# Performance work log

Measured on AMD Instinct MI355X. Metric: run time of the kernel, lower is better.

## Reference

```python
import jax, jax.numpy as jnp
import numpy as np

N_NODES = 100000
N_EDGES = 3200000
D = 256


def setup_inputs() -> dict:
    key = jax.random.key(0)
    k1, k2, k3, k4, k5, k6 = jax.random.split(key, 6)
    embeddings = jax.random.normal(k1, (N_NODES, D), dtype=jnp.float32)
    edge_vals = jax.random.uniform(k2, (N_EDGES,), dtype=jnp.float32)
    # glorot-ish scale for the dense transforms
    scale = 1.0 / np.sqrt(D)
    W1 = jax.random.normal(k3, (D, D), dtype=jnp.float32) * scale
    W2 = jax.random.normal(k4, (D, D), dtype=jnp.float32) * scale
    edge_rows = jax.random.randint(k5, (N_EDGES,), 0, N_NODES, dtype=jnp.int32)
    edge_cols = jax.random.randint(k6, (N_EDGES,), 0, N_NODES, dtype=jnp.int32)
    return {
        "embeddings": embeddings,
        "edge_vals": edge_vals,
        "W1": W1,
        "W2": W2,
        "edge_rows": edge_rows,
        "edge_cols": edge_cols,
    }


def reference(embeddings, edge_vals, W1, W2, edge_rows, edge_cols):
    # SpMM: neighbor_interaction = A @ embeddings, A given as COO (rows, cols, vals)
    gathered = edge_vals[:, None] * embeddings[edge_cols]          # [E, D]
    neighbor = jax.ops.segment_sum(gathered, edge_rows,
                                   num_segments=embeddings.shape[0])  # [N, D]
    # include_self_messages = True branch:
    # self_interaction + neighbor_messages  ==  (emb + neighbor) @ W1
    out = (embeddings + neighbor) @ W1 + (neighbor * embeddings) @ W2
    return out
```

## Files before the change

### kernel.cpp

```cpp
#include <hip/hip_runtime.h>
#include <cstdint>
#include <cstddef>

#define N_NODES 100000
#define N_EDGES 3200000
#define DD 256
#define KK 512
#define MPAD 100096
#define NSCAN 98
#define NGRP 8
#define GRP_ROWS 12500
#define NSLOT 256
#define SLOT_E 12500

typedef __attribute__((ext_vector_type(8))) __bf16 bf16x8;
typedef __attribute__((ext_vector_type(4))) __bf16 bf16x4;
typedef __attribute__((ext_vector_type(4))) float f32x4;

__device__ __forceinline__ void gload_lds16(const void* gsrc, void* lds) {
  __builtin_amdgcn_global_load_lds((const __attribute__((address_space(1))) void*)gsrc,
                                   (__attribute__((address_space(3))) void*)lds,
                                   16, 0, 0);
}


__global__ void conve_kernel(const float* __restrict__ emb, __bf16* __restrict__ embB) {
  int i = blockIdx.x * blockDim.x + threadIdx.x;
  float4 v = ((const float4*)emb)[i];
  bf16x4 o;
  o[0] = (__bf16)v.x; o[1] = (__bf16)v.y; o[2] = (__bf16)v.z; o[3] = (__bf16)v.w;
  ((bf16x4*)embB)[i] = o;
}

__global__ void convw_kernel(const float* __restrict__ W1, const float* __restrict__ W2,
                             __bf16* __restrict__ Wt) {
  int idx = blockIdx.x * blockDim.x + threadIdx.x;
  int n = idx >> 9;
  int k = idx & 511;
  float v = (k < 256) ? W1[k * 256 + n] : W2[(k - 256) * 256 + n];
  Wt[idx] = (__bf16)v;
}


__global__ void zero_ints_kernel(int* __restrict__ p, int n) {
  int i = blockIdx.x * blockDim.x + threadIdx.x;
  if (i < n) p[i] = 0;
}

__global__ void hist_kernel(const int* __restrict__ rows, int* __restrict__ counts, int e) {
  int i = blockIdx.x * blockDim.x + threadIdx.x;
  int stride = gridDim.x * blockDim.x;
  for (; i < e; i += stride) atomicAdd(&counts[rows[i]], 1);
}

__global__ void scan_block_kernel(const int* __restrict__ counts, int* __restrict__ offsets,
                                  int* __restrict__ blockSums, int n) {
  __shared__ int s[1024];
  int t = threadIdx.x;
  int i = blockIdx.x * 1024 + t;
  int v = (i < n) ? counts[i] : 0;
  s[t] = v;
  __syncthreads();
  for (int off = 1; off < 1024; off <<= 1) {
    int x = (t >= off) ? s[t - off] : 0;
    __syncthreads();
    s[t] += x;
    __syncthreads();
  }
  if (i < n) offsets[i + 1] = s[t];
  if (t == 1023) blockSums[blockIdx.x] = s[1023];
}

__global__ void scan_sums_kernel(const int* __restrict__ blockSums, int* __restrict__ blockBase,
                                 int nb, int* __restrict__ offsets) {
  __shared__ int s[128];
  int t = threadIdx.x;
  int v = (t < nb) ? blockSums[t] : 0;
  s[t] = v;
  __syncthreads();
  for (int off = 1; off < 128; off <<= 1) {
    int x = (t >= off) ? s[t - off] : 0;
    __syncthreads();
    s[t] += x;
    __syncthreads();
  }
  if (t < nb) blockBase[t] = s[t] - v;
  if (t == 0) offsets[0] = 0;
}

__global__ void scan_add_kernel(const int* __restrict__ counts, int* __restrict__ offsets,
                                const int* __restrict__ blockBase, int* __restrict__ cursor, int n) {
  int i = blockIdx.x * 1024 + threadIdx.x;
  if (i < n) {
    int incl = offsets[i + 1] + blockBase[blockIdx.x];
    offsets[i + 1] = incl;
    cursor[i] = incl - counts[i];
  }
}

__global__ void bin_kernel(const int* __restrict__ rows, const int* __restrict__ cols,
                           const float* __restrict__ vals, int* __restrict__ cursor,
                           uint2* __restrict__ sedge) {
  const int g = blockIdx.x & (NGRP - 1);
  const int s = blockIdx.x >> 3;
  const int rlo = g * GRP_ROWS;
  const int rhi = rlo + GRP_ROWS;
  const int base = s * SLOT_E;
  for (int i = base + threadIdx.x; i < base + SLOT_E; i += 256) {
    int r = rows[i];
    if (r >= rlo && r < rhi) {
      int pos = atomicAdd(&cursor[r], 1);
      sedge[pos] = make_uint2((unsigned)cols[i], __float_as_uint(vals[i]));
    }
  }
}


__global__ void spmm_fuse_kernel(const __bf16* __restrict__ embB, const int* __restrict__ offsets,
                                 const uint2* __restrict__ sedge, __bf16* __restrict__ X) {
  int gw = (blockIdx.x << 2) + (threadIdx.x >> 6);
  int lane = threadIdx.x & 63;
  bf16x4* xp1 = (bf16x4*)(X + (size_t)gw * KK + 4 * lane);
  bf16x4* xp2 = (bf16x4*)(X + (size_t)gw * KK + DD + 4 * lane);
  if (gw >= N_NODES) {
    bf16x4 z;
    z[0] = (__bf16)0.f; z[1] = (__bf16)0.f; z[2] = (__bf16)0.f; z[3] = (__bf16)0.f;
    *xp1 = z; *xp2 = z;
    return;
  }
  const bf16x4* ev = (const bf16x4*)embB;
  float ax = 0.f, ay = 0.f, az = 0.f, aw = 0.f;
  int e = offsets[gw];
  const int eend = offsets[gw + 1];
  for (; e + 3 < eend; e += 4) {
    uint2 e0 = sedge[e], e1 = sedge[e + 1], e2 = sedge[e + 2], e3 = sedge[e + 3];
    float v0 = __uint_as_float(e0.y), v1 = __uint_as_float(e1.y);
    float v2 = __uint_as_float(e2.y), v3 = __uint_as_float(e3.y);
    bf16x4 x0 = ev[(size_t)e0.x * 64 + lane];
    bf16x4 x1 = ev[(size_t)e1.x * 64 + lane];
    bf16x4 x2 = ev[(size_t)e2.x * 64 + lane];
    bf16x4 x3 = ev[(size_t)e3.x * 64 + lane];
    ax = fmaf(v0, (float)x0[0], ax); ay = fmaf(v0, (float)x0[1], ay);
    az = fmaf(v0, (float)x0[2], az); aw = fmaf(v0, (float)x0[3], aw);
    ax = fmaf(v1, (float)x1[0], ax); ay = fmaf(v1, (float)x1[1], ay);
    az = fmaf(v1, (float)x1[2], az); aw = fmaf(v1, (float)x1[3], aw);
    ax = fmaf(v2, (float)x2[0], ax); ay = fmaf(v2, (float)x2[1], ay);
    az = fmaf(v2, (float)x2[2], az); aw = fmaf(v2, (float)x2[3], aw);
    ax = fmaf(v3, (float)x3[0], ax); ay = fmaf(v3, (float)x3[1], ay);
    az = fmaf(v3, (float)x3[2], az); aw = fmaf(v3, (float)x3[3], aw);
  }
  for (; e < eend; ++e) {
    uint2 ee = sedge[e];
    float v = __uint_as_float(ee.y);
    bf16x4 x = ev[(size_t)ee.x * 64 + lane];
    ax = fmaf(v, (float)x[0], ax); ay = fmaf(v, (float)x[1], ay);
    az = fmaf(v, (float)x[2], az); aw = fmaf(v, (float)x[3], aw);
  }
  bf16x4 er = ev[(size_t)gw * 64 + lane];
  float ex = (float)er[0], ey = (float)er[1], ez = (float)er[2], ew = (float)er[3];
  bf16x4 o1, o2;
  o1[0] = (__bf16)(ex + ax); o1[1] = (__bf16)(ey + ay);
  o1[2] = (__bf16)(ez + az); o1[3] = (__bf16)(ew + aw);
  o2[0] = (__bf16)(ex * ax); o2[1] = (__bf16)(ey * ay);
  o2[2] = (__bf16)(ez * az); o2[3] = (__bf16)(ew * aw);
  *xp1 = o1;
  *xp2 = o2;
}


__global__ __launch_bounds__(256) void gemm_kernel(const __bf16* __restrict__ X,
                                                   const __bf16* __restrict__ Wt,
                                                   float* __restrict__ out) {
  __shared__ __align__(16) __bf16 As[128 * 64];
  __shared__ __align__(16) __bf16 Bs[128 * 64];
  const int t = threadIdx.x;
  const int w = t >> 6, lane = t & 63;
  const int m0 = blockIdx.x * 128;
  const int n0 = blockIdx.y * 128;
  const int wm = (w >> 1) * 64, wn = (w & 1) * 64;
  const int lrow = lane >> 3, lcol = lane & 7;

  f32x4 acc[4][4];
#pragma unroll
  for (int i = 0; i < 4; ++i)
#pragma unroll
    for (int j = 0; j < 4; ++j) {
      f32x4 z = {0.f, 0.f, 0.f, 0.f};
      acc[i][j] = z;
    }

  for (int kt = 0; kt < KK; kt += 64) {
#pragma unroll
    for (int q = 0; q < 4; ++q) {
      const int cbase = w * 256 + q * 64;
      const int arow = m0 + w * 32 + q * 8 + lrow;
      gload_lds16(X + (size_t)arow * KK + kt + lcol * 8, (char*)As + cbase * 16);
      const int brow = n0 + w * 32 + q * 8 + lrow;
      gload_lds16(Wt + (size_t)brow * KK + kt + lcol * 8, (char*)Bs + cbase * 16);
    }
    __syncthreads();
#pragma unroll
    for (int kk = 0; kk < 64; kk += 32) {
      const int ko = kk + (lane >> 4) * 8;
      bf16x8 af[4], bg[4];
#pragma unroll
      for (int i = 0; i < 4; ++i)
        af[i] = *(const bf16x8*)(As + (wm + i * 16 + (lane & 15)) * 64 + ko);
#pragma unroll
      for (int j = 0; j < 4; ++j)
        bg[j] = *(const bf16x8*)(Bs + (wn + j * 16 + (lane & 15)) * 64 + ko);
#pragma unroll
      for (int i = 0; i < 4; ++i)
#pragma unroll
        for (int j = 0; j < 4; ++j)
          acc[i][j] = __builtin_amdgcn_mfma_f32_16x16x32_bf16(af[i], bg[j], acc[i][j], 0, 0, 0);
    }
    __syncthreads();
  }

  const int orow0 = m0 + wm + ((lane >> 4) << 2);
  const int ocol0 = n0 + wn + (lane & 15);
#pragma unroll
  for (int i = 0; i < 4; ++i)
#pragma unroll
    for (int j = 0; j < 4; ++j)
#pragma unroll
      for (int r = 0; r < 4; ++r) {
        const int row = orow0 + i * 16 + r;
        if (row < N_NODES) out[(size_t)row * DD + ocol0 + j * 16] = acc[i][j][r];
      }
}


extern "C" void kernel_launch(void* const* d_in, const int* in_sizes, int n_in,
                              void* d_out, int out_size, void* d_ws, size_t ws_size,
                              hipStream_t stream) {
  const float* emb  = (const float*)d_in[0];
  const float* ev   = (const float*)d_in[1];
  const float* W1   = (const float*)d_in[2];
  const float* W2   = (const float*)d_in[3];
  const int* erows  = (const int*)d_in[4];
  const int* ecols  = (const int*)d_in[5];
  float* out = (float*)d_out;
  char* ws = (char*)d_ws;

  const size_t OFF_X   = 0;
  const size_t OFF_EMB = OFF_X   + (size_t)MPAD * KK * 2;
  const size_t OFF_WT  = OFF_EMB + (size_t)N_NODES * DD * 2;
  const size_t OFF_CNT = OFF_WT  + (size_t)KK * DD * 2;
  const size_t OFF_OFS = OFF_CNT + 401408;
  const size_t OFF_CUR = OFF_OFS + 401408;
  const size_t OFF_BS  = OFF_CUR + 401408;
  const size_t OFF_BB  = OFF_BS  + 4096;
  const size_t OFF_SE  = OFF_BB  + 4096;

  __bf16* X     = (__bf16*)(ws + OFF_X);
  __bf16* embB  = (__bf16*)(ws + OFF_EMB);
  __bf16* Wt    = (__bf16*)(ws + OFF_WT);
  int* counts   = (int*)(ws + OFF_CNT);
  int* offsets  = (int*)(ws + OFF_OFS);
  int* cursor   = (int*)(ws + OFF_CUR);
  int* bsums    = (int*)(ws + OFF_BS);
  int* bbase    = (int*)(ws + OFF_BB);
  uint2* sedge  = (uint2*)(ws + OFF_SE);

  conve_kernel<<<(N_NODES * 64) / 256, 256, 0, stream>>>(emb, embB);
  convw_kernel<<<(KK * DD) / 256, 256, 0, stream>>>(W1, W2, Wt);

  zero_ints_kernel<<<(N_NODES + 255) / 256, 256, 0, stream>>>(counts, N_NODES);
  hist_kernel<<<2048, 256, 0, stream>>>(erows, counts, N_EDGES);
  scan_block_kernel<<<NSCAN, 1024, 0, stream>>>(counts, offsets, bsums, N_NODES);
  scan_sums_kernel<<<1, 128, 0, stream>>>(bsums, bbase, NSCAN, offsets);
  scan_add_kernel<<<NSCAN, 1024, 0, stream>>>(counts, offsets, bbase, cursor, N_NODES);
  bin_kernel<<<NGRP * NSLOT, 256, 0, stream>>>(erows, ecols, ev, cursor, sedge);

  spmm_fuse_kernel<<<MPAD / 4, 256, 0, stream>>>(embB, offsets, sedge, X);

  gemm_kernel<<<dim3(MPAD / 128, 2), 256, 0, stream>>>(X, Wt, out);

  (void)in_sizes; (void)n_in; (void)out_size; (void)ws_size;
}
```

Measured before the change: 770.5 us.

## Fuse SpMM aggregation with the dense GEMM through a swizzled LDS tile

New measurement: 852.6 us. +10.7%, slower.

```diff
diff --git a/kernel.cpp b/kernel.cpp
--- a/kernel.cpp
+++ b/kernel.cpp
@@ -17,12 +17,6 @@
 typedef __attribute__((ext_vector_type(4))) __bf16 bf16x4;
 typedef __attribute__((ext_vector_type(4))) float f32x4;
 
-__device__ __forceinline__ void gload_lds16(const void* gsrc, void* lds) {
-  __builtin_amdgcn_global_load_lds((const __attribute__((address_space(1))) void*)gsrc,
-                                   (__attribute__((address_space(3))) void*)lds,
-                                   16, 0, 0);
-}
-
 
 __global__ void conve_kernel(const float* __restrict__ emb, __bf16* __restrict__ embB) {
   int i = blockIdx.x * blockDim.x + threadIdx.x;
@@ -47,10 +41,16 @@
   if (i < n) p[i] = 0;
 }
 
-__global__ void hist_kernel(const int* __restrict__ rows, int* __restrict__ counts, int e) {
-  int i = blockIdx.x * blockDim.x + threadIdx.x;
-  int stride = gridDim.x * blockDim.x;
-  for (; i < e; i += stride) atomicAdd(&counts[rows[i]], 1);
+__global__ void hist_kernel(const int* __restrict__ rows, int* __restrict__ counts) {
+  const int g = blockIdx.x & (NGRP - 1);
+  const int s = blockIdx.x >> 3;
+  const int rlo = g * GRP_ROWS;
+  const int rhi = rlo + GRP_ROWS;
+  const int base = s * SLOT_E;
+  for (int i = base + threadIdx.x; i < base + SLOT_E; i += 256) {
+    int r = rows[i];
+    if (r >= rlo && r < rhi) atomicAdd(&counts[r], 1);
+  }
 }
 
 __global__ void scan_block_kernel(const int* __restrict__ counts, int* __restrict__ offsets,
@@ -116,118 +116,107 @@
 }
 
 
-__global__ void spmm_fuse_kernel(const __bf16* __restrict__ embB, const int* __restrict__ offsets,
-                                 const uint2* __restrict__ sedge, __bf16* __restrict__ X) {
-  int gw = (blockIdx.x << 2) + (threadIdx.x >> 6);
-  int lane = threadIdx.x & 63;
-  bf16x4* xp1 = (bf16x4*)(X + (size_t)gw * KK + 4 * lane);
-  bf16x4* xp2 = (bf16x4*)(X + (size_t)gw * KK + DD + 4 * lane);
-  if (gw >= N_NODES) {
-    bf16x4 z;
-    z[0] = (__bf16)0.f; z[1] = (__bf16)0.f; z[2] = (__bf16)0.f; z[3] = (__bf16)0.f;
-    *xp1 = z; *xp2 = z;
-    return;
-  }
-  const bf16x4* ev = (const bf16x4*)embB;
-  float ax = 0.f, ay = 0.f, az = 0.f, aw = 0.f;
-  int e = offsets[gw];
-  const int eend = offsets[gw + 1];
-  for (; e + 3 < eend; e += 4) {
-    uint2 e0 = sedge[e], e1 = sedge[e + 1], e2 = sedge[e + 2], e3 = sedge[e + 3];
-    float v0 = __uint_as_float(e0.y), v1 = __uint_as_float(e1.y);
-    float v2 = __uint_as_float(e2.y), v3 = __uint_as_float(e3.y);
-    bf16x4 x0 = ev[(size_t)e0.x * 64 + lane];
-    bf16x4 x1 = ev[(size_t)e1.x * 64 + lane];
-    bf16x4 x2 = ev[(size_t)e2.x * 64 + lane];
-    bf16x4 x3 = ev[(size_t)e3.x * 64 + lane];
-    ax = fmaf(v0, (float)x0[0], ax); ay = fmaf(v0, (float)x0[1], ay);
-    az = fmaf(v0, (float)x0[2], az); aw = fmaf(v0, (float)x0[3], aw);
-    ax = fmaf(v1, (float)x1[0], ax); ay = fmaf(v1, (float)x1[1], ay);
-    az = fmaf(v1, (float)x1[2], az); aw = fmaf(v1, (float)x1[3], aw);
-    ax = fmaf(v2, (float)x2[0], ax); ay = fmaf(v2, (float)x2[1], ay);
-    az = fmaf(v2, (float)x2[2], az); aw = fmaf(v2, (float)x2[3], aw);
-    ax = fmaf(v3, (float)x3[0], ax); ay = fmaf(v3, (float)x3[1], ay);
-    az = fmaf(v3, (float)x3[2], az); aw = fmaf(v3, (float)x3[3], aw);
-  }
-  for (; e < eend; ++e) {
-    uint2 ee = sedge[e];
-    float v = __uint_as_float(ee.y);
-    bf16x4 x = ev[(size_t)ee.x * 64 + lane];
-    ax = fmaf(v, (float)x[0], ax); ay = fmaf(v, (float)x[1], ay);
-    az = fmaf(v, (float)x[2], az); aw = fmaf(v, (float)x[3], aw);
-  }
-  bf16x4 er = ev[(size_t)gw * 64 + lane];
-  float ex = (float)er[0], ey = (float)er[1], ez = (float)er[2], ew = (float)er[3];
-  bf16x4 o1, o2;
-  o1[0] = (__bf16)(ex + ax); o1[1] = (__bf16)(ey + ay);
-  o1[2] = (__bf16)(ez + az); o1[3] = (__bf16)(ew + aw);
-  o2[0] = (__bf16)(ex * ax); o2[1] = (__bf16)(ey * ay);
-  o2[2] = (__bf16)(ez * az); o2[3] = (__bf16)(ew * aw);
-  *xp1 = o1;
-  *xp2 = o2;
-}
-
-
-__global__ __launch_bounds__(256) void gemm_kernel(const __bf16* __restrict__ X,
-                                                   const __bf16* __restrict__ Wt,
-                                                   float* __restrict__ out) {
-  __shared__ __align__(16) __bf16 As[128 * 64];
-  __shared__ __align__(16) __bf16 Bs[128 * 64];
+__global__ __launch_bounds__(256) void spmm_gemm_kernel(
+    const __bf16* __restrict__ embB, const int* __restrict__ offsets,
+    const uint2* __restrict__ sedge, const __bf16* __restrict__ Wt,
+    float* __restrict__ out) {
+  __shared__ __align__(16) char Xs[32 * 1024];
   const int t = threadIdx.x;
   const int w = t >> 6, lane = t & 63;
-  const int m0 = blockIdx.x * 128;
-  const int n0 = blockIdx.y * 128;
-  const int wm = (w >> 1) * 64, wn = (w & 1) * 64;
-  const int lrow = lane >> 3, lcol = lane & 7;
-
-  f32x4 acc[4][4];
-#pragma unroll
-  for (int i = 0; i < 4; ++i)
+  const int m0 = blockIdx.x * 32;
+  const bf16x4* ev = (const bf16x4*)embB;
+
+  for (int rr = 0; rr < 8; ++rr) {
+    const int lr = (w << 3) + rr;
+    const int r = m0 + lr;
+    const int sw = (lr & 7) << 4;
+    bf16x4* q1 = (bf16x4*)(Xs + lr * 1024 + ((lane * 8) ^ sw));
+    bf16x4* q2 = (bf16x4*)(Xs + lr * 1024 + ((512 + lane * 8) ^ sw));
+    if (r >= N_NODES) {
+      bf16x4 z;
+      z[0] = (__bf16)0.f; z[1] = (__bf16)0.f; z[2] = (__bf16)0.f; z[3] = (__bf16)0.f;
+      *q1 = z; *q2 = z;
+      continue;
+    }
+    float ax = 0.f, ay = 0.f, az = 0.f, aw = 0.f;
+    int e = offsets[r];
+    const int eend = offsets[r + 1];
+    for (; e + 3 < eend; e += 4) {
+      uint2 e0 = sedge[e], e1 = sedge[e + 1], e2 = sedge[e + 2], e3 = sedge[e + 3];
+      float v0 = __uint_as_float(e0.y), v1 = __uint_as_float(e1.y);
+      float v2 = __uint_as_float(e2.y), v3 = __uint_as_float(e3.y);
+      bf16x4 x0 = ev[(size_t)e0.x * 64 + lane];
+      bf16x4 x1 = ev[(size_t)e1.x * 64 + lane];
+      bf16x4 x2 = ev[(size_t)e2.x * 64 + lane];
+      bf16x4 x3 = ev[(size_t)e3.x * 64 + lane];
+      ax = fmaf(v0, (float)x0[0], ax); ay = fmaf(v0, (float)x0[1], ay);
+      az = fmaf(v0, (float)x0[2], az); aw = fmaf(v0, (float)x0[3], aw);
+      ax = fmaf(v1, (float)x1[0], ax); ay = fmaf(v1, (float)x1[1], ay);
+      az = fmaf(v1, (float)x1[2], az); aw = fmaf(v1, (float)x1[3], aw);
+      ax = fmaf(v2, (float)x2[0], ax); ay = fmaf(v2, (float)x2[1], ay);
+      az = fmaf(v2, (float)x2[2], az); aw = fmaf(v2, (float)x2[3], aw);
+      ax = fmaf(v3, (float)x3[0], ax); ay = fmaf(v3, (float)x3[1], ay);
+      az = fmaf(v3, (float)x3[2], az); aw = fmaf(v3, (float)x3[3], aw);
+    }
+    for (; e < eend; ++e) {
+      uint2 ee = sedge[e];
+      float v = __uint_as_float(ee.y);
+      bf16x4 x = ev[(size_t)ee.x * 64 + lane];
+      ax = fmaf(v, (float)x[0], ax); ay = fmaf(v, (float)x[1], ay);
+      az = fmaf(v, (float)x[2], az); aw = fmaf(v, (float)x[3], aw);
+    }
+    bf16x4 er = ev[(size_t)r * 64 + lane];
+    float ex = (float)er[0], ey = (float)er[1], ez = (float)er[2], ew = (float)er[3];
+    bf16x4 o1, o2;
+    o1[0] = (__bf16)(ex + ax); o1[1] = (__bf16)(ey + ay);
+    o1[2] = (__bf16)(ez + az); o1[3] = (__bf16)(ew + aw);
+    o2[0] = (__bf16)(ex * ax); o2[1] = (__bf16)(ey * ay);
+    o2[2] = (__bf16)(ez * az); o2[3] = (__bf16)(ew * aw);
+    *q1 = o1;
+    *q2 = o2;
+  }
+  __syncthreads();
+
+  f32x4 acc[2][4];
+#pragma unroll
+  for (int mt = 0; mt < 2; ++mt)
 #pragma unroll
     for (int j = 0; j < 4; ++j) {
       f32x4 z = {0.f, 0.f, 0.f, 0.f};
-      acc[i][j] = z;
-    }
-
-  for (int kt = 0; kt < KK; kt += 64) {
-#pragma unroll
-    for (int q = 0; q < 4; ++q) {
-      const int cbase = w * 256 + q * 64;
-      const int arow = m0 + w * 32 + q * 8 + lrow;
-      gload_lds16(X + (size_t)arow * KK + kt + lcol * 8, (char*)As + cbase * 16);
-      const int brow = n0 + w * 32 + q * 8 + lrow;
-      gload_lds16(Wt + (size_t)brow * KK + kt + lcol * 8, (char*)Bs + cbase * 16);
-    }
-    __syncthreads();
-#pragma unroll
-    for (int kk = 0; kk < 64; kk += 32) {
-      const int ko = kk + (lane >> 4) * 8;
-      bf16x8 af[4], bg[4];
-#pragma unroll
-      for (int i = 0; i < 4; ++i)
-        af[i] = *(const bf16x8*)(As + (wm + i * 16 + (lane & 15)) * 64 + ko);
+      acc[mt][j] = z;
+    }
+  const int n0w = w << 6;
+  const int l15 = lane & 15, lhi = lane >> 4;
+#pragma unroll 4
+  for (int ks = 0; ks < 16; ++ks) {
+    const int kk = ks << 5;
+    bf16x8 af[2], bg[4];
+#pragma unroll
+    for (int mt = 0; mt < 2; ++mt) {
+      const int ar = (mt << 4) + l15;
+      int off = ar * 1024 + (kk << 1) + (lhi << 4);
+      off ^= (ar & 7) << 4;
+      af[mt] = *(const bf16x8*)(Xs + off);
+    }
+#pragma unroll
+    for (int j = 0; j < 4; ++j)
+      bg[j] = *(const bf16x8*)(Wt + (size_t)(n0w + (j << 4) + l15) * KK + kk + (lhi << 3));
+#pragma unroll
+    for (int mt = 0; mt < 2; ++mt)
 #pragma unroll
       for (int j = 0; j < 4; ++j)
-        bg[j] = *(const bf16x8*)(Bs + (wn + j * 16 + (lane & 15)) * 64 + ko);
-#pragma unroll
-      for (int i = 0; i < 4; ++i)
-#pragma unroll
-        for (int j = 0; j < 4; ++j)
-          acc[i][j] = __builtin_amdgcn_mfma_f32_16x16x32_bf16(af[i], bg[j], acc[i][j], 0, 0, 0);
-    }
-    __syncthreads();
-  }
-
-  const int orow0 = m0 + wm + ((lane >> 4) << 2);
-  const int ocol0 = n0 + wn + (lane & 15);
-#pragma unroll
-  for (int i = 0; i < 4; ++i)
+        acc[mt][j] = __builtin_amdgcn_mfma_f32_16x16x32_bf16(af[mt], bg[j], acc[mt][j], 0, 0, 0);
+  }
+
+  const int ocol0 = n0w + l15;
+#pragma unroll
+  for (int mt = 0; mt < 2; ++mt)
 #pragma unroll
     for (int j = 0; j < 4; ++j)
 #pragma unroll
-      for (int r = 0; r < 4; ++r) {
-        const int row = orow0 + i * 16 + r;
-        if (row < N_NODES) out[(size_t)row * DD + ocol0 + j * 16] = acc[i][j][r];
+      for (int r2 = 0; r2 < 4; ++r2) {
+        const int row = m0 + (mt << 4) + (lhi << 2) + r2;
+        if (row < N_NODES) out[(size_t)row * DD + ocol0 + (j << 4)] = acc[mt][j][r2];
       }
 }
 
@@ -244,8 +233,7 @@
   float* out = (float*)d_out;
   char* ws = (char*)d_ws;
 
-  const size_t OFF_X   = 0;
-  const size_t OFF_EMB = OFF_X   + (size_t)MPAD * KK * 2;
+  const size_t OFF_EMB = 0;
   const size_t OFF_WT  = OFF_EMB + (size_t)N_NODES * DD * 2;
   const size_t OFF_CNT = OFF_WT  + (size_t)KK * DD * 2;
   const size_t OFF_OFS = OFF_CNT + 401408;
@@ -254,7 +242,6 @@
   const size_t OFF_BB  = OFF_BS  + 4096;
   const size_t OFF_SE  = OFF_BB  + 4096;
 
-  __bf16* X     = (__bf16*)(ws + OFF_X);
   __bf16* embB  = (__bf16*)(ws + OFF_EMB);
   __bf16* Wt    = (__bf16*)(ws + OFF_WT);
   int* counts   = (int*)(ws + OFF_CNT);
@@ -268,15 +255,13 @@
   convw_kernel<<<(KK * DD) / 256, 256, 0, stream>>>(W1, W2, Wt);
 
   zero_ints_kernel<<<(N_NODES + 255) / 256, 256, 0, stream>>>(counts, N_NODES);
-  hist_kernel<<<2048, 256, 0, stream>>>(erows, counts, N_EDGES);
+  hist_kernel<<<NGRP * NSLOT, 256, 0, stream>>>(erows, counts);
   scan_block_kernel<<<NSCAN, 1024, 0, stream>>>(counts, offsets, bsums, N_NODES);
   scan_sums_kernel<<<1, 128, 0, stream>>>(bsums, bbase, NSCAN, offsets);
   scan_add_kernel<<<NSCAN, 1024, 0, stream>>>(counts, offsets, bbase, cursor, N_NODES);
   bin_kernel<<<NGRP * NSLOT, 256, 0, stream>>>(erows, ecols, ev, cursor, sedge);
 
-  spmm_fuse_kernel<<<MPAD / 4, 256, 0, stream>>>(embB, offsets, sedge, X);
-
-  gemm_kernel<<<dim3(MPAD / 128, 2), 256, 0, stream>>>(X, Wt, out);
+  spmm_gemm_kernel<<<MPAD / 32, 256, 0, stream>>>(embB, offsets, sedge, Wt, out);
 
   (void)in_sizes; (void)n_in; (void)out_size; (void)ws_size;
 }
```
